# Kernel optimization log

Measured on AMD Instinct MI355X. Metric: run time of the kernel, lower is better.

The kernel has to match this reference:

```python
import jax, jax.numpy as jnp
import numpy as np

B, L, D = 8, 512, 256


def hard_sigmoid(x):
    # Keras 1.x default inner_activation for LSTM gates
    return jnp.clip(0.2 * x + 0.5, 0.0, 1.0)


def lstm_step(x_t, h, c, W, U, b):
    # gates in Keras order: i, f, g(candidate), o
    z = x_t @ W + h @ U + b  # (B, 4D)
    i, f, g, o = jnp.split(z, 4, axis=-1)
    i = hard_sigmoid(i)
    f = hard_sigmoid(f)
    g = jnp.tanh(g)
    o = hard_sigmoid(o)
    c_new = f * c + i * g
    h_new = o * jnp.tanh(c_new)
    return h_new, c_new


def setup_inputs() -> dict:
    key = jax.random.key(0)
    ks = jax.random.split(key, 10)
    s = 1.0 / np.sqrt(D)
    x = jax.random.normal(ks[0], (B, L, D), dtype=jnp.float32)
    W_r = jax.random.normal(ks[1], (D, 4 * D), dtype=jnp.float32) * s
    U_r = jax.random.normal(ks[2], (D, 4 * D), dtype=jnp.float32) * s
    b_r = jnp.zeros((4 * D,), dtype=jnp.float32)
    W_w = jax.random.normal(ks[3], (D, 4 * D), dtype=jnp.float32) * s
    U_w = jax.random.normal(ks[4], (D, 4 * D), dtype=jnp.float32) * s
    b_w = jnp.zeros((4 * D,), dtype=jnp.float32)
    W_c = jax.random.normal(ks[5], (2 * D, D), dtype=jnp.float32) * s
    b_c = jnp.zeros((D,), dtype=jnp.float32)
    return {"x": x, "W_r": W_r, "U_r": U_r, "b_r": b_r,
            "W_w": W_w, "U_w": U_w, "b_w": b_w, "W_c": W_c, "b_c": b_c}


def reference(x, W_r, U_r, b_r, W_w, U_w, b_w, W_c, b_c):
    Bb, Ll, Dd = x.shape
    h0 = jnp.zeros((Bb, Dd), dtype=x.dtype)

    # --- reader LSTM (return_sequences=True), eq. 1 ---
    def reader_step(carry, x_t):
        h, c = carry
        h, c = lstm_step(x_t, h, c, W_r, U_r, b_r)
        return (h, c), h

    _, o_seq = jax.lax.scan(reader_step, (h0, h0), jnp.swapaxes(x, 0, 1))  # (L, B, D)

    # --- compose-and-write loop, eqs. 2-6; mem_0 = x ---
    def write_step(carry, o_t):
        mem, h, c = carry  # mem: (B, L, D)
        z = jax.nn.softmax(jnp.einsum('bd,bld->bl', o_t, mem), axis=-1)  # (B, L)
        m_rt = jnp.einsum('bl,bld->bd', z, mem)                           # (B, D)
        c_t = jnp.concatenate([o_t, m_rt], axis=-1) @ W_c + b_c          # linear composer
        h_new, c_new = lstm_step(c_t, h, c, W_w, U_w, b_w)
        mem_new = mem * (1.0 - z[..., None]) + h_new[:, None, :] * z[..., None]
        return (mem_new, h_new, c_new), h_new

    (_, _, _), h_seq = jax.lax.scan(write_step, (x, h0, h0), o_seq)
    # return_mode == 'last_output'
    return h_seq[-1]
```

## Files before the change

### kernel.cpp

```cpp
#include <hip/hip_runtime.h>
#include <math.h>

#define BB 8
#define LL 512
#define DD 256
#define NG4 1024
#define WGB 32
#define WR 16
#define WU 8
#define MLD 264

typedef __attribute__((ext_vector_type(4))) float f32x4;

static const size_t OFF_XW    = 0;
static const size_t OFF_F     = OFF_XW + (size_t)BB*LL*NG4;
static const size_t OFF_BMW   = OFF_F + (size_t)DD*NG4;
static const size_t OFF_B2    = OFF_BMW + (size_t)DD*NG4;
static const size_t OFF_HR    = OFF_B2 + NG4;
static const size_t OFF_HW    = OFF_HR + (size_t)2*BB*DD;
static const size_t OFF_PMAX  = OFF_HW + (size_t)BB*DD;
static const size_t OFF_PSUM  = OFF_PMAX + (size_t)BB*WGB;
static const size_t OFF_PM    = OFF_PSUM + (size_t)BB*WGB;
static const size_t OFF_FLAGS = OFF_PM + (size_t)BB*WGB*DD;
static const size_t TOTAL_WS  = OFF_FLAGS + BB*WGB;

__device__ __forceinline__ float hsig(float x) {
    return fminf(fmaxf(0.2f*x + 0.5f, 0.0f), 1.0f);
}

__device__ __forceinline__ void st_coh(float* p, float v) {
    __hip_atomic_store(p, v, __ATOMIC_RELAXED, __HIP_MEMORY_SCOPE_AGENT);
}
__device__ __forceinline__ float ld_coh(const float* p) {
    return __hip_atomic_load(p, __ATOMIC_RELAXED, __HIP_MEMORY_SCOPE_AGENT);
}
__device__ __forceinline__ void st_coh_u(unsigned* p, unsigned v) {
    __hip_atomic_store(p, v, __ATOMIC_RELAXED, __HIP_MEMORY_SCOPE_AGENT);
}
__device__ __forceinline__ unsigned ld_coh_u(const unsigned* p) {
    return __hip_atomic_load(p, __ATOMIC_RELAXED, __HIP_MEMORY_SCOPE_AGENT);
}

__device__ __forceinline__ void ld_pm8(
    const f32x4* p0, const f32x4* p1, const f32x4* p2, const f32x4* p3,
    const f32x4* p4, const f32x4* p5, const f32x4* p6, const f32x4* p7,
    f32x4& a0, f32x4& a1, f32x4& a2, f32x4& a3,
    f32x4& a4, f32x4& a5, f32x4& a6, f32x4& a7)
{
    asm volatile(
        "global_load_dwordx4 %0, %8, off sc0 sc1\n\t"
        "global_load_dwordx4 %1, %9, off sc0 sc1\n\t"
        "global_load_dwordx4 %2, %10, off sc0 sc1\n\t"
        "global_load_dwordx4 %3, %11, off sc0 sc1\n\t"
        "global_load_dwordx4 %4, %12, off sc0 sc1\n\t"
        "global_load_dwordx4 %5, %13, off sc0 sc1\n\t"
        "global_load_dwordx4 %6, %14, off sc0 sc1\n\t"
        "global_load_dwordx4 %7, %15, off sc0 sc1\n\t"
        "s_waitcnt vmcnt(0)"
        : "=&v"(a0), "=&v"(a1), "=&v"(a2), "=&v"(a3),
          "=&v"(a4), "=&v"(a5), "=&v"(a6), "=&v"(a7)
        : "v"(p0), "v"(p1), "v"(p2), "v"(p3),
          "v"(p4), "v"(p5), "v"(p6), "v"(p7)
        : "memory");
}

template<int TM, int TN, int TK>
__global__ void __launch_bounds__(256) gemm_nn(
    const float* __restrict__ A, int lda,
    const float* __restrict__ Bmat, int ldb,
    const float* __restrict__ bias,
    float* __restrict__ C, int ldc,
    int M, int N, int K)
{
    __shared__ float As[TK][TM];
    __shared__ float Bs[TK][TN];
    const int m0 = blockIdx.y * TM, n0 = blockIdx.x * TN;
    const int tid = threadIdx.x;
    const int tx = tid % (TN/4);
    const int ty = tid / (TN/4);
    float acc[4][4] = {};
    for (int k0 = 0; k0 < K; k0 += TK) {
        {
            const int e = tid*4;
            const int m = e / TK, k = e % TK;
            const float4 v = *reinterpret_cast<const float4*>(&A[(size_t)(m0+m)*lda + k0 + k]);
            As[k+0][m] = v.x; As[k+1][m] = v.y; As[k+2][m] = v.z; As[k+3][m] = v.w;
        }
        {
            const int e = tid*4;
            const int k = e / TN, n = e % TN;
            const float4 v = *reinterpret_cast<const float4*>(&Bmat[(size_t)(k0+k)*ldb + n0 + n]);
            Bs[k][n+0] = v.x; Bs[k][n+1] = v.y; Bs[k][n+2] = v.z; Bs[k][n+3] = v.w;
        }
        __syncthreads();
        #pragma unroll
        for (int kk = 0; kk < TK; ++kk) {
            float a[4], bv[4];
            #pragma unroll
            for (int i = 0; i < 4; ++i) a[i] = As[kk][ty*4+i];
            #pragma unroll
            for (int j = 0; j < 4; ++j) bv[j] = Bs[kk][tx*4+j];
            #pragma unroll
            for (int i = 0; i < 4; ++i)
                #pragma unroll
                for (int j = 0; j < 4; ++j) acc[i][j] += a[i]*bv[j];
        }
        __syncthreads();
    }
    #pragma unroll
    for (int i = 0; i < 4; ++i) {
        const int m = m0 + ty*4 + i;
        #pragma unroll
        for (int j = 0; j < 4; ++j) {
            const int n = n0 + tx*4 + j;
            C[(size_t)m*ldc + n] = acc[i][j] + (bias ? bias[n] : 0.0f);
        }
    }
}

__global__ void __launch_bounds__(256) b2_kernel(
    const float* __restrict__ bc, const float* __restrict__ Ww,
    const float* __restrict__ bw, float* __restrict__ B2)
{
    const int n = blockIdx.x*256 + threadIdx.x;
    float a = bw[n];
    for (int k = 0; k < DD; ++k) a += bc[k]*Ww[(size_t)k*NG4 + n];
    B2[n] = a;
}

__global__ void __launch_bounds__(256) fused_kernel(
    const float* __restrict__ XW, const float* __restrict__ Fw,
    const float* __restrict__ Bm, const float* __restrict__ B2,
    const float* __restrict__ Ur, const float* __restrict__ Uw,
    const float* __restrict__ x,
    float* __restrict__ HR, float* __restrict__ HWb,
    float* __restrict__ PMAX, float* __restrict__ PSUM, float* __restrict__ PM,
    unsigned* __restrict__ flags, float* __restrict__ out)
{
    extern __shared__ float sm[];
    float* Urs  = sm;
    float* Uws  = Urs + 8192;
    float* Fs   = Uws + 8192;
    float* Bms  = Fs + 8192;
    float* mems = Bms + 8192;
    float* hr2  = mems + WR*MLD;
    float* hw   = hr2 + 512;
    float* ms   = hw + 256;
    float* zredR= ms + 256;
    float* zredW= zredR + 256;
    float* red4 = zredW + 256;
    float* xws  = red4 + 1024;
    float* b2s  = xws + 32;
    float* zrs  = b2s + 32;
    float* zws  = zrs + 32;
    float* fwS  = zws + 32;
    float* d1   = fwS + 32;
    float* zp   = d1 + 16;
    float* esx  = zp + 16;
    float* wv   = esx + 16;
    float* wsum = wv + 16;
    float* cr   = wsum + 8;
    float* cw   = cr + 8;
    float* misc = cw + 8;

    const int b   = (int)blockIdx.x & 7;
    const int wg  = (int)blockIdx.x >> 3;
    const int tid = threadIdx.x;
    const int R0  = wg*WR;
    const int U0  = wg*WU;
    const int gc32 = (tid>>3)*DD + U0 + (tid&7);

    for (int it = 0; it < 32; ++it) {
        const int e = it*256 + tid;
        const int k = e >> 5, cl = e & 31;
        const int gc = (cl>>3)*DD + U0 + (cl&7);
        Urs[k*32+cl] = Ur[(size_t)k*NG4 + gc];
        Uws[k*32+cl] = Uw[(size_t)k*NG4 + gc];
        Fs [k*32+cl] = Fw[(size_t)k*NG4 + gc];
        Bms[k*32+cl] = Bm[(size_t)k*NG4 + gc];
    }
    if (tid < 32) b2s[tid] = B2[gc32];
    for (int r = 0; r < WR; ++r)
        mems[r*MLD + tid] = x[((size_t)b*LL + R0 + r)*DD + tid];
    {
        const size_t base = (size_t)b*LL*NG4;
        const float zi = XW[base + tid];
        const float zg = XW[base + 512 + tid];
        const float zo = XW[base + 768 + tid];
        const float c0 = hsig(zi)*tanhf(zg);
        hr2[tid] = hsig(zo)*tanhf(c0);
        hr2[256 + tid] = 0.f;
        if (tid >= U0 && tid < U0+WU) cr[tid-U0] = c0;
    }
    if (tid < 16) { zp[tid] = 0.f; d1[tid] = 0.f; esx[tid] = 0.f; }
    if (tid < 8)  cw[tid] = 0.f;
    if (tid < 4)  misc[tid] = 0.f;
    __syncthreads();

    unsigned* flb = flags + b*WGB;

    for (int s = 0; s <= LL; ++s) {
        const bool doW = (s >= 1);
        float* hrN_s = hr2 + (s&1)*256;
        float* hrO_s = hr2 + ((s+1)&1)*256;

        float hw_r = 0.f;
        if (s >= 2) hw_r = ld_coh(&HWb[b*DD + tid]);
        hw[tid] = hw_r;
        __syncthreads();

        {
            float v = hrO_s[tid]*hw_r;
            #pragma unroll
            for (int off = 32; off; off >>= 1) v += __shfl_xor(v, off);
            if ((tid & 63) == 0) wsum[tid>>6] = v;
        }
        __syncthreads();

        if (doW && tid < 16) {
            const float d2v = wsum[0]+wsum[1]+wsum[2]+wsum[3];
            const float zpv = zp[tid];
            const float sc  = (1.f - zpv)*d1[tid] + zpv*d2v;
            float m = sc;
            #pragma unroll
            for (int off = 8; off; off >>= 1) m = fmaxf(m, __shfl_xor(m, off, 16));
            const float e = __expf(sc - m);
            esx[tid] = e;
            wv[tid]  = e*(1.f - zpv);
            float sum = e, bp = e*zpv;
            #pragma unroll
            for (int off = 8; off; off >>= 1) {
                sum += __shfl_xor(sum, off, 16);
                bp  += __shfl_xor(bp,  off, 16);
            }
            if (tid == 0) {
                misc[2] = bp;
                st_coh(&PMAX[b*WGB + wg], m);
                st_coh(&PSUM[b*WGB + wg], sum);
            }
        }
        __syncthreads();

        if (doW) {
            float p = misc[2]*hw_r;
            #pragma unroll
            for (int r = 0; r < WR; ++r) p += wv[r]*mems[r*MLD + tid];
            st_coh(&PM[((size_t)b*WGB + wg)*DD + tid], p);
        }

        asm volatile("s_waitcnt vmcnt(0)" ::: "memory");
        __syncthreads();
        if (tid == 0) st_coh_u(&flb[wg], 2u*(unsigned)s + 1u);
        if (s >= 2) {
            #pragma unroll
            for (int r = 0; r < WR; ++r) {
                const float z = zp[r];
                float* mp = &mems[r*MLD + tid];
                *mp = *mp*(1.f - z) + hw_r*z;
            }
        }
        if (tid < 64) {
            const unsigned target = 2u*(unsigned)s + 1u;
            unsigned v;
            do { v = ld_coh_u(&flb[tid & 31]); } while (!__all(v >= target));
        }
        __syncthreads();

        float hrN_r = 0.f;
        if (s >= 1 && s <= 511) hrN_r = ld_coh(&HR[((size_t)(s&1))*BB*DD + b*DD + tid]);
        float xw_r = 0.f;
        if (s <= 510 && tid < 32) xw_r = XW[((size_t)b*LL + s + 1)*NG4 + gc32];
        float pmx_r = 0.f, ps_r = 0.f;
        if (doW && tid < 32) {
            pmx_r = ld_coh(&PMAX[b*WGB + tid]);
            ps_r  = ld_coh(&PSUM[b*WGB + tid]);
        }
        f32x4 a0,a1,a2,a3,a4,a5,a6,a7;
        const int w0 = tid >> 6, dq = tid & 63;
        if (doW) {
            const float* pmb = PM + (size_t)b*WGB*DD;
            ld_pm8((const f32x4*)(pmb + (w0+ 0)*DD) + dq, (const f32x4*)(pmb + (w0+ 4)*DD) + dq,
                   (const f32x4*)(pmb + (w0+ 8)*DD) + dq, (const f32x4*)(pmb + (w0+12)*DD) + dq,
                   (const f32x4*)(pmb + (w0+16)*DD) + dq, (const f32x4*)(pmb + (w0+20)*DD) + dq,
                   (const f32x4*)(pmb + (w0+24)*DD) + dq, (const f32x4*)(pmb + (w0+28)*DD) + dq,
                   a0,a1,a2,a3,a4,a5,a6,a7);
        }
        if (s >= 1 && s <= 511) hrN_s[tid] = hrN_r;
        if (s <= 510 && tid < 32) xws[tid] = xw_r;
        __syncthreads();

        if (doW) {
            if (tid < 32) {
                float g = pmx_r;
                #pragma unroll
                for (int off = 16; off; off >>= 1) g = fmaxf(g, __shfl_xor(g, off, 32));
                const float fw = __expf(pmx_r - g);
                float S = ps_r*fw;
                #pragma unroll
                for (int off = 16; off; off >>= 1) S += __shfl_xor(S, off, 32);
                fwS[tid] = fw;
                if (tid == 0)  misc[1] = 1.f/S;
                if (tid == wg) misc[0] = fw/S;
            }
            __syncthreads();
            {
                f32x4 acc = a0*fwS[w0];
                acc += a1*fwS[w0+4];  acc += a2*fwS[w0+8];
                acc += a3*fwS[w0+12]; acc += a4*fwS[w0+16];
                acc += a5*fwS[w0+20]; acc += a6*fwS[w0+24];
                acc += a7*fwS[w0+28];
                *(f32x4*)(red4 + w0*DD + dq*4) = acc;
            }
            __syncthreads();
            ms[tid] = (red4[tid] + red4[DD+tid] + red4[2*DD+tid] + red4[3*DD+tid]) * misc[1];
            if (tid < 16) zp[tid] = esx[tid]*misc[0];
            __syncthreads();
            {
                const int kc = tid >> 5, cl = tid & 31, k0 = kc*32;
                float a = 0.f;
                #pragma unroll 8
                for (int k = k0; k < k0+32; ++k)
                    a += hw[k]*Uws[k*32+cl] + hrO_s[k]*Fs[k*32+cl] + ms[k]*Bms[k*32+cl];
                zredW[tid] = a;
            }
            __syncthreads();
            if (tid < 32) {
                float z = b2s[tid];
                #pragma unroll
                for (int q = 0; q < 8; ++q) z += zredW[q*32 + tid];
                zws[tid] = z;
            }
            __syncthreads();
            if (tid < 8) {
                const float ig = hsig(zws[tid]);
                const float fg = hsig(zws[8+tid]);
                const float gg = tanhf(zws[16+tid]);
                const float og = hsig(zws[24+tid]);
                const float c  = fg*cw[tid] + ig*gg;
                cw[tid] = c;
                const float h = og*tanhf(c);
                st_coh(&HWb[b*DD + U0 + tid], h);
                if (s == LL) out[b*DD + U0 + tid] = h;
            }
        }

        if (s <= 510) {
            const int kc = tid >> 5, cl = tid & 31, k0 = kc*32;
            float a = 0.f;
            #pragma unroll 8
            for (int k = k0; k < k0+32; ++k) a += hrN_s[k]*Urs[k*32+cl];
            zredR[tid] = a;
        }
        __syncthreads();
        if (s <= 510 && tid < 32) {
            float z = xws[tid];
            #pragma unroll
            for (int q = 0; q < 8; ++q) z += zredR[q*32 + tid];
            zrs[tid] = z;
        }
        __syncthreads();
        if (s <= 510 && tid < 8) {
            const float ig = hsig(zrs[tid]);
            const float fg = hsig(zrs[8+tid]);
            const float gg = tanhf(zrs[16+tid]);
            const float og = hsig(zrs[24+tid]);
            const float c  = fg*cr[tid] + ig*gg;
            cr[tid] = c;
            st_coh(&HR[((size_t)((s+1)&1))*BB*DD + b*DD + U0 + tid], og*tanhf(c));
        }
        if (s < LL) {
            const int r = tid >> 4, j = tid & 15;
            float a = 0.f;
            const float* mrow = mems + r*MLD;
            #pragma unroll 4
            for (int d = j; d < DD; d += 16) a += hrN_s[d]*mrow[d];
            #pragma unroll
            for (int off = 8; off; off >>= 1) a += __shfl_down(a, off, 16);
            if (j == 0) d1[r] = a;
        }

        if (s < LL) {
            asm volatile("s_waitcnt vmcnt(0)" ::: "memory");
            __syncthreads();
            if (tid == 0) st_coh_u(&flb[wg], 2u*(unsigned)s + 2u);
            if (tid < 64) {
                const unsigned target = 2u*(unsigned)s + 2u;
                unsigned v;
                do { v = ld_coh_u(&flb[tid & 31]); } while (!__all(v >= target));
            }
            __syncthreads();
        }
    }
}

extern "C" void kernel_launch(void* const* d_in, const int* in_sizes, int n_in,
                              void* d_out, int out_size, void* d_ws, size_t ws_size,
                              hipStream_t stream) {
    const float* x   = (const float*)d_in[0];
    const float* W_r = (const float*)d_in[1];
    const float* U_r = (const float*)d_in[2];
    const float* b_r = (const float*)d_in[3];
    const float* W_w = (const float*)d_in[4];
    const float* U_w = (const float*)d_in[5];
    const float* b_w = (const float*)d_in[6];
    const float* W_c = (const float*)d_in[7];
    const float* b_c = (const float*)d_in[8];
    (void)in_sizes; (void)n_in;

    if (ws_size < TOTAL_WS * sizeof(float)) return;

    float* ws   = (float*)d_ws;
    float* XW   = ws + OFF_XW;
    float* Fmat = ws + OFF_F;
    float* Bmw  = ws + OFF_BMW;
    float* B2   = ws + OFF_B2;
    float* HR   = ws + OFF_HR;
    float* HWb  = ws + OFF_HW;
    float* PMAX = ws + OFF_PMAX;
    float* PSUM = ws + OFF_PSUM;
    float* PM   = ws + OFF_PM;
    unsigned* flags = (unsigned*)(ws + OFF_FLAGS);

    const int FUSED_LDS = 39808 * 4;
    hipFuncSetAttribute((const void*)fused_kernel, hipFuncAttributeMaxDynamicSharedMemorySize, FUSED_LDS);

    hipMemsetAsync(flags, 0, BB*WGB*sizeof(unsigned), stream);

    dim3 blk(256);
    gemm_nn<64,64,16><<<dim3(NG4/64, (BB*LL)/64), blk, 0, stream>>>(
        x, DD, W_r, NG4, b_r, XW, NG4, BB*LL, NG4, DD);
    gemm_nn<64,64,16><<<dim3(NG4/64, DD/64), blk, 0, stream>>>(
        W_c, DD, W_w, NG4, nullptr, Fmat, NG4, DD, NG4, DD);
    gemm_nn<64,64,16><<<dim3(NG4/64, DD/64), blk, 0, stream>>>(
        W_c + (size_t)DD*DD, DD, W_w, NG4, nullptr, Bmw, NG4, DD, NG4, DD);
    b2_kernel<<<dim3(NG4/256), blk, 0, stream>>>(b_c, W_w, b_w, B2);
    fused_kernel<<<dim3(BB*WGB), blk, FUSED_LDS, stream>>>(
        XW, Fmat, Bmw, B2, U_r, U_w, x, HR, HWb, PMAX, PSUM, PM, flags, (float*)d_out);
}
```

Measured before the change: 4.373 ms.

## Use counter barrier, precompute partial dot products, overlap work with spin-waits

Replaces the per-workgroup flag array barrier with a single atomic counter per batch that one thread polls with s_sleep. Each workgroup now publishes the partial dot product of its new write-LSTM hidden slice with the reader hidden state (RHO). This removes the block-wide reduction and two __syncthreads at the start of each step. Independent work (the Uw/F partial gate products, the d1 memory scores, the XW prefetch) is moved to run between the barrier arrive and wait, and the reader and writer gate reductions are merged into one phase. The risks are contention on the shared atomic counter and a more intricate ordering of cross-block dependencies.

```diff
diff --git a/kernel.cpp b/kernel.cpp
--- a/kernel.cpp
+++ b/kernel.cpp
@@ -20,9 +20,10 @@
 static const size_t OFF_HW    = OFF_HR + (size_t)2*BB*DD;
 static const size_t OFF_PMAX  = OFF_HW + (size_t)BB*DD;
 static const size_t OFF_PSUM  = OFF_PMAX + (size_t)BB*WGB;
-static const size_t OFF_PM    = OFF_PSUM + (size_t)BB*WGB;
+static const size_t OFF_RHO   = OFF_PSUM + (size_t)BB*WGB;
+static const size_t OFF_PM    = OFF_RHO + (size_t)BB*WGB;
 static const size_t OFF_FLAGS = OFF_PM + (size_t)BB*WGB*DD;
-static const size_t TOTAL_WS  = OFF_FLAGS + BB*WGB;
+static const size_t TOTAL_WS  = OFF_FLAGS + BB*32;
 
 __device__ __forceinline__ float hsig(float x) {
     return fminf(fmaxf(0.2f*x + 0.5f, 0.0f), 1.0f);
@@ -33,9 +34,6 @@
 }
 __device__ __forceinline__ float ld_coh(const float* p) {
     return __hip_atomic_load(p, __ATOMIC_RELAXED, __HIP_MEMORY_SCOPE_AGENT);
-}
-__device__ __forceinline__ void st_coh_u(unsigned* p, unsigned v) {
-    __hip_atomic_store(p, v, __ATOMIC_RELAXED, __HIP_MEMORY_SCOPE_AGENT);
 }
 __device__ __forceinline__ unsigned ld_coh_u(const unsigned* p) {
     return __hip_atomic_load(p, __ATOMIC_RELAXED, __HIP_MEMORY_SCOPE_AGENT);
@@ -134,7 +132,8 @@
     const float* __restrict__ Ur, const float* __restrict__ Uw,
     const float* __restrict__ x,
     float* __restrict__ HR, float* __restrict__ HWb,
-    float* __restrict__ PMAX, float* __restrict__ PSUM, float* __restrict__ PM,
+    float* __restrict__ PMAX, float* __restrict__ PSUM, float* __restrict__ RHO,
+    float* __restrict__ PM,
     unsigned* __restrict__ flags, float* __restrict__ out)
 {
     extern __shared__ float sm[];
@@ -158,8 +157,7 @@
     float* zp   = d1 + 16;
     float* esx  = zp + 16;
     float* wv   = esx + 16;
-    float* wsum = wv + 16;
-    float* cr   = wsum + 8;
+    float* cr   = wv + 16;
     float* cw   = cr + 8;
     float* misc = cw + 8;
 
@@ -197,46 +195,46 @@
     if (tid < 4)  misc[tid] = 0.f;
     __syncthreads();
 
-    unsigned* flb = flags + b*WGB;
+    unsigned* flb = &flags[b*32];
 
     for (int s = 0; s <= LL; ++s) {
         const bool doW = (s >= 1);
         float* hrN_s = hr2 + (s&1)*256;
         float* hrO_s = hr2 + ((s+1)&1)*256;
 
-        float hw_r = 0.f;
-        if (s >= 2) hw_r = ld_coh(&HWb[b*DD + tid]);
+        float xw_r = 0.f;
+        if (s <= LL-2 && tid < 32) xw_r = XW[((size_t)b*LL + s + 1)*NG4 + gc32];
+        float hw_r = 0.f, rho_r = 0.f;
+        if (s >= 2) {
+            hw_r = ld_coh(&HWb[b*DD + tid]);
+            if (tid < 32) rho_r = ld_coh(&RHO[b*WGB + tid]);
+        }
         hw[tid] = hw_r;
-        __syncthreads();
-
-        {
-            float v = hrO_s[tid]*hw_r;
-            #pragma unroll
-            for (int off = 32; off; off >>= 1) v += __shfl_xor(v, off);
-            if ((tid & 63) == 0) wsum[tid>>6] = v;
-        }
-        __syncthreads();
-
-        if (doW && tid < 16) {
-            const float d2v = wsum[0]+wsum[1]+wsum[2]+wsum[3];
-            const float zpv = zp[tid];
-            const float sc  = (1.f - zpv)*d1[tid] + zpv*d2v;
-            float m = sc;
-            #pragma unroll
-            for (int off = 8; off; off >>= 1) m = fmaxf(m, __shfl_xor(m, off, 16));
-            const float e = __expf(sc - m);
-            esx[tid] = e;
-            wv[tid]  = e*(1.f - zpv);
-            float sum = e, bp = e*zpv;
-            #pragma unroll
-            for (int off = 8; off; off >>= 1) {
-                sum += __shfl_xor(sum, off, 16);
-                bp  += __shfl_xor(bp,  off, 16);
-            }
-            if (tid == 0) {
-                misc[2] = bp;
-                st_coh(&PMAX[b*WGB + wg], m);
-                st_coh(&PSUM[b*WGB + wg], sum);
+
+        if (tid < 32) {
+            float d2 = rho_r;
+            #pragma unroll
+            for (int off = 16; off; off >>= 1) d2 += __shfl_xor(d2, off, 32);
+            if (doW && tid < 16) {
+                const float zpv = zp[tid];
+                const float sc  = (1.f - zpv)*d1[tid] + zpv*d2;
+                float m = sc;
+                #pragma unroll
+                for (int off = 8; off; off >>= 1) m = fmaxf(m, __shfl_xor(m, off, 16));
+                const float e = __expf(sc - m);
+                esx[tid] = e;
+                wv[tid]  = e*(1.f - zpv);
+                float sum = e, bp = e*zpv;
+                #pragma unroll
+                for (int off = 8; off; off >>= 1) {
+                    sum += __shfl_xor(sum, off, 16);
+                    bp  += __shfl_xor(bp,  off, 16);
+                }
+                if (tid == 0) {
+                    misc[2] = bp;
+                    st_coh(&PMAX[b*WGB + wg], m);
+                    st_coh(&PSUM[b*WGB + wg], sum);
+                }
             }
         }
         __syncthreads();
@@ -250,7 +248,8 @@
 
         asm volatile("s_waitcnt vmcnt(0)" ::: "memory");
         __syncthreads();
-        if (tid == 0) st_coh_u(&flb[wg], 2u*(unsigned)s + 1u);
+        if (tid == 0)
+            __hip_atomic_fetch_add(flb, 1u, __ATOMIC_RELAXED, __HIP_MEMORY_SCOPE_AGENT);
         if (s >= 2) {
             #pragma unroll
             for (int r = 0; r < WR; ++r) {
@@ -259,17 +258,22 @@
                 *mp = *mp*(1.f - z) + hw_r*z;
             }
         }
-        if (tid < 64) {
-            const unsigned target = 2u*(unsigned)s + 1u;
-            unsigned v;
-            do { v = ld_coh_u(&flb[tid & 31]); } while (!__all(v >= target));
+        if (doW) {
+            const int kc = tid >> 5, cl = tid & 31, k0 = kc*32;
+            float a = 0.f;
+            #pragma unroll 8
+            for (int k = k0; k < k0+32; ++k)
+                a += hw[k]*Uws[k*32+cl] + hrO_s[k]*Fs[k*32+cl];
+            zredW[tid] = a;
+        }
+        if (tid == 0) {
+            const unsigned target = 64u*(unsigned)s + 32u;
+            while (ld_coh_u(flb) < target) __builtin_amdgcn_s_sleep(1);
         }
         __syncthreads();
 
         float hrN_r = 0.f;
-        if (s >= 1 && s <= 511) hrN_r = ld_coh(&HR[((size_t)(s&1))*BB*DD + b*DD + tid]);
-        float xw_r = 0.f;
-        if (s <= 510 && tid < 32) xw_r = XW[((size_t)b*LL + s + 1)*NG4 + gc32];
+        if (s >= 1 && s <= LL-1) hrN_r = ld_coh(&HR[((size_t)(s&1))*BB*DD + b*DD + tid]);
         float pmx_r = 0.f, ps_r = 0.f;
         if (doW && tid < 32) {
             pmx_r = ld_coh(&PMAX[b*WGB + tid]);
@@ -285,66 +289,23 @@
                    (const f32x4*)(pmb + (w0+24)*DD) + dq, (const f32x4*)(pmb + (w0+28)*DD) + dq,
                    a0,a1,a2,a3,a4,a5,a6,a7);
         }
-        if (s >= 1 && s <= 511) hrN_s[tid] = hrN_r;
-        if (s <= 510 && tid < 32) xws[tid] = xw_r;
-        __syncthreads();
-
-        if (doW) {
-            if (tid < 32) {
-                float g = pmx_r;
-                #pragma unroll
-                for (int off = 16; off; off >>= 1) g = fmaxf(g, __shfl_xor(g, off, 32));
-                const float fw = __expf(pmx_r - g);
-                float S = ps_r*fw;
-                #pragma unroll
-                for (int off = 16; off; off >>= 1) S += __shfl_xor(S, off, 32);
-                fwS[tid] = fw;
-                if (tid == 0)  misc[1] = 1.f/S;
-                if (tid == wg) misc[0] = fw/S;
-            }
-            __syncthreads();
-            {
-                f32x4 acc = a0*fwS[w0];
-                acc += a1*fwS[w0+4];  acc += a2*fwS[w0+8];
-                acc += a3*fwS[w0+12]; acc += a4*fwS[w0+16];
-                acc += a5*fwS[w0+20]; acc += a6*fwS[w0+24];
-                acc += a7*fwS[w0+28];
-                *(f32x4*)(red4 + w0*DD + dq*4) = acc;
-            }
-            __syncthreads();
-            ms[tid] = (red4[tid] + red4[DD+tid] + red4[2*DD+tid] + red4[3*DD+tid]) * misc[1];
-            if (tid < 16) zp[tid] = esx[tid]*misc[0];
-            __syncthreads();
-            {
-                const int kc = tid >> 5, cl = tid & 31, k0 = kc*32;
-                float a = 0.f;
-                #pragma unroll 8
-                for (int k = k0; k < k0+32; ++k)
-                    a += hw[k]*Uws[k*32+cl] + hrO_s[k]*Fs[k*32+cl] + ms[k]*Bms[k*32+cl];
-                zredW[tid] = a;
-            }
-            __syncthreads();
-            if (tid < 32) {
-                float z = b2s[tid];
-                #pragma unroll
-                for (int q = 0; q < 8; ++q) z += zredW[q*32 + tid];
-                zws[tid] = z;
-            }
-            __syncthreads();
-            if (tid < 8) {
-                const float ig = hsig(zws[tid]);
-                const float fg = hsig(zws[8+tid]);
-                const float gg = tanhf(zws[16+tid]);
-                const float og = hsig(zws[24+tid]);
-                const float c  = fg*cw[tid] + ig*gg;
-                cw[tid] = c;
-                const float h = og*tanhf(c);
-                st_coh(&HWb[b*DD + U0 + tid], h);
-                if (s == LL) out[b*DD + U0 + tid] = h;
-            }
-        }
-
-        if (s <= 510) {
+        if (s >= 1 && s <= LL-1) hrN_s[tid] = hrN_r;
+        if (s <= LL-2 && tid < 32) xws[tid] = xw_r;
+        __syncthreads();
+
+        if (doW && tid < 32) {
+            float g = pmx_r;
+            #pragma unroll
+            for (int off = 16; off; off >>= 1) g = fmaxf(g, __shfl_xor(g, off, 32));
+            const float fw = __expf(pmx_r - g);
+            float S = ps_r*fw;
+            #pragma unroll
+            for (int off = 16; off; off >>= 1) S += __shfl_xor(S, off, 32);
+            fwS[tid] = fw;
+            if (tid == 0)  misc[1] = 1.f/S;
+            if (tid == wg) misc[0] = fw/S;
+        }
+        if (s <= LL-2) {
             const int kc = tid >> 5, cl = tid & 31, k0 = kc*32;
             float a = 0.f;
             #pragma unroll 8
@@ -352,14 +313,64 @@
             zredR[tid] = a;
         }
         __syncthreads();
-        if (s <= 510 && tid < 32) {
-            float z = xws[tid];
-            #pragma unroll
-            for (int q = 0; q < 8; ++q) z += zredR[q*32 + tid];
-            zrs[tid] = z;
-        }
-        __syncthreads();
-        if (s <= 510 && tid < 8) {
+
+        if (doW) {
+            f32x4 acc = a0*fwS[w0];
+            acc += a1*fwS[w0+4];  acc += a2*fwS[w0+8];
+            acc += a3*fwS[w0+12]; acc += a4*fwS[w0+16];
+            acc += a5*fwS[w0+20]; acc += a6*fwS[w0+24];
+            acc += a7*fwS[w0+28];
+            *(f32x4*)(red4 + w0*DD + dq*4) = acc;
+        }
+        __syncthreads();
+        if (doW) {
+            ms[tid] = (red4[tid] + red4[DD+tid] + red4[2*DD+tid] + red4[3*DD+tid]) * misc[1];
+            if (tid < 16) zp[tid] = esx[tid]*misc[0];
+        }
+        __syncthreads();
+        if (doW) {
+            const int kc = tid >> 5, cl = tid & 31, k0 = kc*32;
+            float a = zredW[tid];
+            #pragma unroll 8
+            for (int k = k0; k < k0+32; ++k) a += ms[k]*Bms[k*32+cl];
+            zredW[tid] = a;
+        }
+        __syncthreads();
+        if (tid < 32) {
+            if (doW) {
+                float z = b2s[tid];
+                #pragma unroll
+                for (int q = 0; q < 8; ++q) z += zredW[q*32 + tid];
+                zws[tid] = z;
+            }
+            if (s <= LL-2) {
+                float z = xws[tid];
+                #pragma unroll
+                for (int q = 0; q < 8; ++q) z += zredR[q*32 + tid];
+                zrs[tid] = z;
+            }
+        }
+        __syncthreads();
+
+        if (doW && tid < 8) {
+            const float ig = hsig(zws[tid]);
+            const float fg = hsig(zws[8+tid]);
+            const float gg = tanhf(zws[16+tid]);
+            const float og = hsig(zws[24+tid]);
+            const float c  = fg*cw[tid] + ig*gg;
+            cw[tid] = c;
+            const float h = og*tanhf(c);
+            st_coh(&HWb[b*DD + U0 + tid], h);
+            if (s < LL) {
+                float rr = h * hrN_s[U0 + tid];
+                rr += __shfl_down(rr, 4, 8);
+                rr += __shfl_down(rr, 2, 8);
+                rr += __shfl_down(rr, 1, 8);
+                if (tid == 0) st_coh(&RHO[b*WGB + wg], rr);
+            }
+            if (s == LL) out[b*DD + U0 + tid] = h;
+        }
+        if (s <= LL-2 && tid < 8) {
             const float ig = hsig(zrs[tid]);
             const float fg = hsig(zrs[8+tid]);
             const float gg = tanhf(zrs[16+tid]);
@@ -368,25 +379,25 @@
             cr[tid] = c;
             st_coh(&HR[((size_t)((s+1)&1))*BB*DD + b*DD + U0 + tid], og*tanhf(c));
         }
-        if (s < LL) {
-            const int r = tid >> 4, j = tid & 15;
-            float a = 0.f;
-            const float* mrow = mems + r*MLD;
-            #pragma unroll 4
-            for (int d = j; d < DD; d += 16) a += hrN_s[d]*mrow[d];
-            #pragma unroll
-            for (int off = 8; off; off >>= 1) a += __shfl_down(a, off, 16);
-            if (j == 0) d1[r] = a;
-        }
 
         if (s < LL) {
             asm volatile("s_waitcnt vmcnt(0)" ::: "memory");
             __syncthreads();
-            if (tid == 0) st_coh_u(&flb[wg], 2u*(unsigned)s + 2u);
-            if (tid < 64) {
-                const unsigned target = 2u*(unsigned)s + 2u;
-                unsigned v;
-                do { v = ld_coh_u(&flb[tid & 31]); } while (!__all(v >= target));
+            if (tid == 0)
+                __hip_atomic_fetch_add(flb, 1u, __ATOMIC_RELAXED, __HIP_MEMORY_SCOPE_AGENT);
+            {
+                const int r = tid >> 4, j = tid & 15;
+                float a = 0.f;
+                const float* mrow = mems + r*MLD;
+                #pragma unroll 4
+                for (int d = j; d < DD; d += 16) a += hrN_s[d]*mrow[d];
+                #pragma unroll
+                for (int off = 8; off; off >>= 1) a += __shfl_down(a, off, 16);
+                if (j == 0) d1[r] = a;
+            }
+            if (tid == 0) {
+                const unsigned target = 64u*(unsigned)s + 64u;
+                while (ld_coh_u(flb) < target) __builtin_amdgcn_s_sleep(1);
             }
             __syncthreads();
         }
@@ -418,13 +429,14 @@
     float* HWb  = ws + OFF_HW;
     float* PMAX = ws + OFF_PMAX;
     float* PSUM = ws + OFF_PSUM;
+    float* RHO  = ws + OFF_RHO;
     float* PM   = ws + OFF_PM;
     unsigned* flags = (unsigned*)(ws + OFF_FLAGS);
 
-    const int FUSED_LDS = 39808 * 4;
+    const int FUSED_LDS = 39800 * 4;
     hipFuncSetAttribute((const void*)fused_kernel, hipFuncAttributeMaxDynamicSharedMemorySize, FUSED_LDS);
 
-    hipMemsetAsync(flags, 0, BB*WGB*sizeof(unsigned), stream);
+    hipMemsetAsync(flags, 0, BB*32*sizeof(unsigned), stream);
 
     dim3 blk(256);
     gemm_nn<64,64,16><<<dim3(NG4/64, (BB*LL)/64), blk, 0, stream>>>(
@@ -435,5 +447,5 @@
         W_c + (size_t)DD*DD, DD, W_w, NG4, nullptr, Bmw, NG4, DD, NG4, DD);
     b2_kernel<<<dim3(NG4/256), blk, 0, stream>>>(b_c, W_w, b_w, B2);
     fused_kernel<<<dim3(BB*WGB), blk, FUSED_LDS, stream>>>(
-        XW, Fmat, Bmw, B2, U_r, U_w, x, HR, HWb, PMAX, PSUM, PM, flags, (float*)d_out);
-}
+        XW, Fmat, Bmw, B2, U_r, U_w, x, HR, HWb, PMAX, PSUM, RHO, PM, flags, (float*)d_out);
+}
```

Measured after the change: 3.984 ms. 8.9% less time.
